# Kernel optimization log

Measured on AMD Instinct MI355X. Metric: run time of the kernel, lower is better.

The kernel has to match this reference:

```python
import jax, jax.numpy as jnp
import numpy as np

HIDDEN = 1024
INTER = 2048
NUM_EXPERTS = 8
TOP_K = 2
GROUP_SIZE = 128
TOKENS = 4096


def _dequant_int4(packed, scale, group_size):
    # packed: [E, N, K//2] ints in [0,256) holding two uint4 nibbles (low | high<<4)
    # scale:  [E, N, K//group_size] float32
    E, N, Kh = packed.shape
    K = 2 * Kh
    low = packed & 0xF
    high = (packed >> 4) & 0xF
    # interleave: even K positions = low nibble, odd = high nibble
    q = jnp.stack([low, high], axis=-1).reshape(E, N, K) - 8  # int4 values in [-8,7]
    q = q.astype(jnp.float32).reshape(E, N, K // group_size, group_size)
    w = q * scale[..., None]
    return w.reshape(E, N, K)


def setup_inputs() -> dict:
    key = jax.random.key(0)
    k1, k2, k3, k4, k5, k6 = jax.random.split(key, 6)
    x = jax.random.normal(k1, (TOKENS, HIDDEN), dtype=jnp.float32)
    router_w = jax.random.normal(k2, (NUM_EXPERTS, HIDDEN), dtype=jnp.float32) * 0.02
    w1 = jax.random.randint(k3, (NUM_EXPERTS, 2 * INTER, HIDDEN // 2), 0, 256, dtype=jnp.int32)
    w1_scale = jax.random.uniform(k4, (NUM_EXPERTS, 2 * INTER, HIDDEN // GROUP_SIZE), dtype=jnp.float32) * 0.05
    w2 = jax.random.randint(k5, (NUM_EXPERTS, HIDDEN, INTER // 2), 0, 256, dtype=jnp.int32)
    w2_scale = jax.random.uniform(k6, (NUM_EXPERTS, HIDDEN, INTER // GROUP_SIZE), dtype=jnp.float32) * 0.05
    return {"x": x, "router_w": router_w, "w1": w1, "w1_scale": w1_scale, "w2": w2, "w2_scale": w2_scale}


def reference(x, router_w, w1, w1_scale, w2, w2_scale):
    # Router: topk then softmax over the top-k logits
    scores = x @ router_w.T                                 # [T, E]
    top_w, top_i = jax.lax.top_k(scores, TOP_K)             # [T, K]
    top_w = jax.nn.softmax(top_w, axis=-1).astype(jnp.float32)

    # Dequantize int4 grouped weights once
    w1_deq = _dequant_int4(w1, w1_scale, GROUP_SIZE)        # [E, 2I, H]
    w2_deq = _dequant_int4(w2, w2_scale, GROUP_SIZE)        # [E, H, I]

    out = jnp.zeros_like(x)
    for e in range(NUM_EXPERTS):
        # per-token routing weight for expert e (0 if not routed)
        ge = jnp.sum(top_w * (top_i == e), axis=-1)         # [T]
        h = x @ w1_deq[e].T                                  # [T, 2I]
        gate, up = h[:, :INTER], h[:, INTER:]
        a = jax.nn.silu(gate) * up                           # SwiGLU
        y = a @ w2_deq[e].T                                  # [T, H]
        out = out + ge[:, None] * y
    return out
```

## Files before the change

kernel.cpp:

```cpp
#include <hip/hip_runtime.h>
#include <hip/hip_bf16.h>

#define HIDDEN 1024
#define INTER 2048
#define NE 8
#define GS 128
#define TOKENS 4096
#define MAXROWS 9216
#define MAXTILES 72
#define MAXT256 40

typedef __bf16 bf16x8 __attribute__((ext_vector_type(8)));
typedef float f32x4 __attribute__((ext_vector_type(4)));

#define OFF_TOPKI 0u
#define OFF_TOPKW 32768u
#define OFF_CTRL  65536u
#define OFF_TOK   66048u
#define OFF_SLOT  102912u
#define OFF_TILE  135680u
#define OFF_T256  136192u
#define OFF_V256  136448u
#define OFF_XB    139776u
#define OFF_A     8530432u
#define OFF_Y0    46279168u
#define OFF_Y1    (OFF_Y0 + 18874368u)

__device__ __forceinline__ unsigned short f2bf(float f) {
  union { float f; unsigned int u; } v; v.f = f;
  unsigned int r = (v.u + 0x7FFFu + ((v.u >> 16) & 1u)) >> 16;
  return (unsigned short)r;
}
__device__ __forceinline__ float bf2f(unsigned int u) {
  union { unsigned int u; float f; } v; v.u = u << 16;
  return v.f;
}
__device__ __forceinline__ unsigned int pack2(unsigned short lo, unsigned short hi) {
  return (unsigned int)lo | ((unsigned int)hi << 16);
}

typedef const __attribute__((address_space(1))) unsigned int GAS;
typedef __attribute__((address_space(3))) unsigned int LAS;
__device__ __forceinline__ void gload16(const unsigned short* g, unsigned short* l) {
  __builtin_amdgcn_global_load_lds((GAS*)g, (LAS*)l, 16, 0, 0);
}

__device__ __forceinline__ uint4 deq8(int4 p, float s, float c) {
  unsigned int pv[4] = { (unsigned int)p.x, (unsigned int)p.y,
                         (unsigned int)p.z, (unsigned int)p.w };
  unsigned int ov[4];
#pragma unroll
  for (int j = 0; j < 4; j++) {
    unsigned int v = pv[j];
    float flo = __uint_as_float(0x43000000u | ((v & 15u) << 16));
    float fhi = __uint_as_float(0x43000000u | ((v << 12) & 0x000F0000u));
    float lo = __builtin_fmaf(flo, s, c);
    float hi = __builtin_fmaf(fhi, s, c);
    unsigned int pk;
    asm("v_cvt_pk_bf16_f32 %0, %1, %2" : "=v"(pk) : "v"(lo), "v"(hi));
    ov[j] = pk;
  }
  uint4 o; o.x = ov[0]; o.y = ov[1]; o.z = ov[2]; o.w = ov[3];
  return o;
}

__global__ __launch_bounds__(256) void k_prep(const float* __restrict__ x,
    const float* __restrict__ rw, int* __restrict__ topki, float* __restrict__ topkw,
    unsigned short* __restrict__ xb) {
  int bid = blockIdx.x, tid = threadIdx.x;
  if (bid == 1024) {
    uint2 z; z.x = 0u; z.y = 0u;
    *reinterpret_cast<uint2*>(xb + (size_t)TOKENS * HIDDEN + tid * 4) = z;
    return;
  }
  int wave = tid >> 6, lane = tid & 63;
  int t = bid * 4 + wave;
  const float* xr = x + (size_t)t * HIDDEN;
  float acc[NE];
#pragma unroll
  for (int e = 0; e < NE; e++) acc[e] = 0.f;
#pragma unroll
  for (int j = 0; j < 4; j++) {
    int col = j * 256 + lane * 4;
    float4 xv = *reinterpret_cast<const float4*>(xr + col);
    uint2 o;
    o.x = pack2(f2bf(xv.x), f2bf(xv.y));
    o.y = pack2(f2bf(xv.z), f2bf(xv.w));
    *reinterpret_cast<uint2*>(xb + (size_t)t * HIDDEN + col) = o;
#pragma unroll
    for (int e = 0; e < NE; e++) {
      float4 wv = *reinterpret_cast<const float4*>(rw + e * HIDDEN + col);
      acc[e] += xv.x * wv.x + xv.y * wv.y + xv.z * wv.z + xv.w * wv.w;
    }
  }
#pragma unroll
  for (int e = 0; e < NE; e++) {
    float v = acc[e];
    for (int off = 32; off > 0; off >>= 1) v += __shfl_down(v, off, 64);
    acc[e] = v;
  }
  if (lane == 0) {
    int b0 = 0; float s0 = acc[0];
#pragma unroll
    for (int e = 1; e < NE; e++) if (acc[e] > s0) { s0 = acc[e]; b0 = e; }
    int b1 = -1; float s1 = -3.0e38f;
#pragma unroll
    for (int e = 0; e < NE; e++) if (e != b0 && acc[e] > s1) { s1 = acc[e]; b1 = e; }
    float w0 = 1.f / (1.f + __expf(s1 - s0));
    topki[t * 2] = b0; topki[t * 2 + 1] = b1;
    topkw[t * 2] = w0; topkw[t * 2 + 1] = 1.f - w0;
  }
}

__global__ __launch_bounds__(256) void k_route2(const int* __restrict__ topki,
    int* __restrict__ ctrl, int* __restrict__ tok, int* __restrict__ slots,
    int* __restrict__ tilemap, int* __restrict__ tile256, int* __restrict__ valid256) {
  __shared__ int h[NE], off[NE], cnt[NE];
  int tid = threadIdx.x;
  if (tid < NE) h[tid] = 0;
  __syncthreads();
  for (int i = tid; i < TOKENS * 2; i += 256) atomicAdd(&h[topki[i]], 1);
  __syncthreads();
  if (tid == 0) {
    int run = 0, t = 0, t2 = 0;
    for (int e = 0; e < NE; e++) {
      int c = h[e];
      ctrl[e] = c; ctrl[16 + e] = run; off[e] = run;
      int pc = (c + 127) & ~127;
      int m = pc >> 7;
      for (int mt = 0; mt < m; mt++) tilemap[t++] = (e << 20) | (run + mt * 128);
      int n2 = (m + 1) >> 1;
      for (int i2 = 0; i2 < n2; i2++) {
        int st = i2 * 256;
        if (st + 256 > pc) st = (pc >= 256) ? (pc - 256) : 0;
        tile256[t2] = (e << 20) | (run + st);
        int v = pc - st; valid256[t2] = (v < 256) ? v : 256;
        t2++;
      }
      run += pc;
    }
    ctrl[24] = run; ctrl[25] = t; ctrl[26] = t2;
  }
  __syncthreads();
#pragma unroll
  for (int e = 0; e < NE; e++) {
    int c = h[e], pc = (c + 127) & ~127;
    for (int i = c + tid; i < pc; i += 256) tok[off[e] + i] = -1;
  }
  if (tid < NE) cnt[tid] = off[tid];
  __syncthreads();
  for (int i = tid; i < TOKENS * 2; i += 256) {
    int e = topki[i];
    int p = atomicAdd(&cnt[e], 1);
    tok[p] = i >> 1;
    slots[i] = p;
  }
}

__global__ __launch_bounds__(256) void k_gemm1(
    const unsigned short* __restrict__ xb, const int* __restrict__ w1,
    const float* __restrict__ w1s, const int* __restrict__ ctrl,
    const int* __restrict__ tilemap, const int* __restrict__ tok,
    unsigned short* __restrict__ a_out) {
  __shared__ unsigned short sA[128 * 32];
  __shared__ unsigned short sBg[64 * 32];
  __shared__ unsigned short sBu[64 * 32];
  int bid = blockIdx.x, tid = threadIdx.x;
  int nt = bid & 31, tile = bid >> 5;
  if (tile >= ctrl[25]) return;
  int tm = tilemap[tile];
  int e = tm >> 20, row0 = tm & 0xFFFFF;
  int n0 = nt * 64;
  int wave = tid >> 6, lane = tid & 63;
  int ln = lane & 15, quad = lane >> 4;
  int wr = (wave & 1) * 64, wc = (wave >> 1) * 32;

  int srow = tid >> 2;
  int gcb = (tid & 3) ^ ((srow >> 1) & 3);
  int scol = gcb * 8;
  int t0 = tok[row0 + srow];
  int t1 = tok[row0 + 64 + srow];
  const unsigned short* gA0 = xb + (size_t)(t0 < 0 ? TOKENS : t0) * HIDDEN + scol;
  const unsigned short* gA1 = xb + (size_t)(t1 < 0 ? TOKENS : t1) * HIDDEN + scol;
  const int* gPg = w1 + (((size_t)e * 4096 + n0 + srow) << 9) + gcb * 4;
  const int* gPu = gPg + ((size_t)2048 << 9);
  const float* sWg = w1s + ((size_t)e * 4096 + n0 + srow) * 8;
  const float* sWu = sWg + 2048 * 8;
  unsigned short* lA0 = sA + tid * 8;
  unsigned short* lA1 = sA + 64 * 32 + tid * 8;
  unsigned short* lBg = sBg + tid * 8;
  unsigned short* lBu = sBu + tid * 8;

  f32x4 aG[4][2] = {}, aU[4][2] = {};
  for (int g = 0; g < 8; g++) {
    float sg_ = sWg[g], su_ = sWu[g];
    float cg = -136.f * sg_, cu = -136.f * su_;
#pragma unroll
    for (int kk = 0; kk < 4; kk++) {
      int k0 = g * 128 + kk * 32;
      __syncthreads();
      gload16(gA0 + k0, lA0);
      gload16(gA1 + k0, lA1);
      int4 pg = *reinterpret_cast<const int4*>(gPg + (k0 >> 1));
      int4 pu = *reinterpret_cast<const int4*>(gPu + (k0 >> 1));
      *reinterpret_cast<uint4*>(lBg) = deq8(pg, sg_, cg);
      *reinterpret_cast<uint4*>(lBu) = deq8(pu, su_, cu);
      __syncthreads();
      bf16x8 af[4], bg[2], bu[2];
#pragma unroll
      for (int m = 0; m < 4; m++) {
        int ar = wr + m * 16 + ln;
        af[m] = *reinterpret_cast<const bf16x8*>(&sA[ar * 32 + (quad ^ ((ar >> 1) & 3)) * 8]);
      }
#pragma unroll
      for (int n = 0; n < 2; n++) {
        int br = wc + n * 16 + ln;
        int bo = br * 32 + (quad ^ ((br >> 1) & 3)) * 8;
        bg[n] = *reinterpret_cast<const bf16x8*>(&sBg[bo]);
        bu[n] = *reinterpret_cast<const bf16x8*>(&sBu[bo]);
      }
#pragma unroll
      for (int m = 0; m < 4; m++)
#pragma unroll
        for (int n = 0; n < 2; n++) {
          aG[m][n] = __builtin_amdgcn_mfma_f32_16x16x32_bf16(af[m], bg[n], aG[m][n], 0, 0, 0);
          aU[m][n] = __builtin_amdgcn_mfma_f32_16x16x32_bf16(af[m], bu[n], aU[m][n], 0, 0, 0);
        }
    }
  }
#pragma unroll
  for (int m = 0; m < 4; m++)
#pragma unroll
    for (int n = 0; n < 2; n++) {
      int col = n0 + wc + n * 16 + ln;
#pragma unroll
      for (int r = 0; r < 4; r++) {
        float g = aG[m][n][r], u = aU[m][n][r];
        float act = (g / (1.f + __expf(-g))) * u;
        int row = row0 + wr + m * 16 + quad * 4 + r;
        a_out[(size_t)row * INTER + col] = f2bf(act);
      }
    }
}

__global__ __launch_bounds__(256) void k_gemm2(
    const unsigned short* __restrict__ a_in, const int* __restrict__ w2,
    const float* __restrict__ w2s, const int* __restrict__ ctrl,
    const int* __restrict__ tilemap, unsigned short* __restrict__ y) {
  __shared__ unsigned short sA[128 * 32];
  __shared__ unsigned short sB[128 * 32];
  int bid = blockIdx.x, tid = threadIdx.x;
  int kp = bid & 1, nt = (bid >> 1) & 7, tile = bid >> 4;
  if (tile >= ctrl[25]) return;
  int tm = tilemap[tile];
  int e = tm >> 20, row0 = tm & 0xFFFFF;
  int n0 = nt * 128;
  int wave = tid >> 6, lane = tid & 63;
  int ln = lane & 15, quad = lane >> 4;
  int wr = (wave & 1) * 64, wc = (wave >> 1) * 64;

  int srow = tid >> 2;
  int gcb = (tid & 3) ^ ((srow >> 1) & 3);
  int scol = gcb * 8;
  int kbase = kp * (INTER / 2);
  const unsigned short* gA0 = a_in + (size_t)(row0 + srow) * INTER + kbase + scol;
  const unsigned short* gA1 = gA0 + (size_t)64 * INTER;
  const int* gP0 = w2 + ((size_t)e * 1024 + n0 + srow) * 1024 + (kbase >> 1) + gcb * 4;
  const int* gP1 = gP0 + (size_t)64 * 1024;
  const float* sW0 = w2s + ((size_t)e * 1024 + n0 + srow) * 16 + kp * 8;
  const float* sW1 = sW0 + 64 * 16;
  unsigned short* lA0 = sA + tid * 8;
  unsigned short* lA1 = sA + 64 * 32 + tid * 8;
  unsigned short* lB0 = sB + tid * 8;
  unsigned short* lB1 = sB + 64 * 32 + tid * 8;

  f32x4 acc[4][4] = {};
  for (int g = 0; g < 8; g++) {
    float s0_ = sW0[g], s1_ = sW1[g];
    float c0 = -136.f * s0_, c1 = -136.f * s1_;
#pragma unroll
    for (int kk = 0; kk < 4; kk++) {
      int k0 = g * 128 + kk * 32;
      __syncthreads();
      gload16(gA0 + k0, lA0);
      gload16(gA1 + k0, lA1);
      int4 p0 = *reinterpret_cast<const int4*>(gP0 + (k0 >> 1));
      int4 p1 = *reinterpret_cast<const int4*>(gP1 + (k0 >> 1));
      *reinterpret_cast<uint4*>(lB0) = deq8(p0, s0_, c0);
      *reinterpret_cast<uint4*>(lB1) = deq8(p1, s1_, c1);
      __syncthreads();
      bf16x8 af[4], bf_[4];
#pragma unroll
      for (int m = 0; m < 4; m++) {
        int ar = wr + m * 16 + ln;
        af[m] = *reinterpret_cast<const bf16x8*>(&sA[ar * 32 + (quad ^ ((ar >> 1) & 3)) * 8]);
      }
#pragma unroll
      for (int n = 0; n < 4; n++) {
        int br = wc + n * 16 + ln;
        bf_[n] = *reinterpret_cast<const bf16x8*>(&sB[br * 32 + (quad ^ ((br >> 1) & 3)) * 8]);
      }
#pragma unroll
      for (int m = 0; m < 4; m++)
#pragma unroll
        for (int n = 0; n < 4; n++)
          acc[m][n] = __builtin_amdgcn_mfma_f32_16x16x32_bf16(af[m], bf_[n], acc[m][n], 0, 0, 0);
    }
  }
  unsigned short* yk = y + (size_t)kp * MAXROWS * HIDDEN;
#pragma unroll
  for (int m = 0; m < 4; m++)
#pragma unroll
    for (int n = 0; n < 4; n++) {
      int col = n0 + wc + n * 16 + ln;
#pragma unroll
      for (int r = 0; r < 4; r++) {
        int row = row0 + wr + m * 16 + quad * 4 + r;
        yk[(size_t)row * HIDDEN + col] = f2bf(acc[m][n][r]);
      }
    }
}

__global__ __launch_bounds__(256) void k_combine(const unsigned short* __restrict__ y,
    const int* __restrict__ slots, const float* __restrict__ topkw,
    float* __restrict__ out) {
  int t = blockIdx.x;
  int c = threadIdx.x * 4;
  int s0 = slots[t * 2], s1 = slots[t * 2 + 1];
  float g0 = topkw[t * 2], g1 = topkw[t * 2 + 1];
  const unsigned short* y1 = y + (size_t)MAXROWS * HIDDEN;
  uint2 a0 = *reinterpret_cast<const uint2*>(y  + (size_t)s0 * HIDDEN + c);
  uint2 a1 = *reinterpret_cast<const uint2*>(y1 + (size_t)s0 * HIDDEN + c);
  uint2 b0 = *reinterpret_cast<const uint2*>(y  + (size_t)s1 * HIDDEN + c);
  uint2 b1 = *reinterpret_cast<const uint2*>(y1 + (size_t)s1 * HIDDEN + c);
  float4 o;
  o.x = g0 * (bf2f(a0.x & 0xffffu) + bf2f(a1.x & 0xffffu))
      + g1 * (bf2f(b0.x & 0xffffu) + bf2f(b1.x & 0xffffu));
  o.y = g0 * (bf2f(a0.x >> 16) + bf2f(a1.x >> 16))
      + g1 * (bf2f(b0.x >> 16) + bf2f(b1.x >> 16));
  o.z = g0 * (bf2f(a0.y & 0xffffu) + bf2f(a1.y & 0xffffu))
      + g1 * (bf2f(b0.y & 0xffffu) + bf2f(b1.y & 0xffffu));
  o.w = g0 * (bf2f(a0.y >> 16) + bf2f(a1.y >> 16))
      + g1 * (bf2f(b0.y >> 16) + bf2f(b1.y >> 16));
  *reinterpret_cast<float4*>(out + (size_t)t * HIDDEN + c) = o;
}

extern "C" void kernel_launch(void* const* d_in, const int* in_sizes, int n_in,
                              void* d_out, int out_size, void* d_ws, size_t ws_size,
                              hipStream_t stream) {
  const float* x   = (const float*)d_in[0];
  const float* rw  = (const float*)d_in[1];
  const int*   w1  = (const int*)d_in[2];
  const float* w1s = (const float*)d_in[3];
  const int*   w2  = (const int*)d_in[4];
  const float* w2s = (const float*)d_in[5];
  float* out = (float*)d_out;
  char* ws = (char*)d_ws;

  int*   topki = (int*)(ws + OFF_TOPKI);
  float* topkw = (float*)(ws + OFF_TOPKW);
  int*   ctrl  = (int*)(ws + OFF_CTRL);
  int*   tok   = (int*)(ws + OFF_TOK);
  int*   slots = (int*)(ws + OFF_SLOT);
  int*   tilemap = (int*)(ws + OFF_TILE);
  int*   tile256 = (int*)(ws + OFF_T256);
  int*   valid256 = (int*)(ws + OFF_V256);
  unsigned short* xb  = (unsigned short*)(ws + OFF_XB);
  unsigned short* a   = (unsigned short*)(ws + OFF_A);
  unsigned short* y   = (unsigned short*)(ws + OFF_Y0);

  k_prep<<<1025, 256, 0, stream>>>(x, rw, topki, topkw, xb);
  k_route2<<<1, 256, 0, stream>>>(topki, ctrl, tok, slots, tilemap, tile256, valid256);
  k_gemm1<<<32 * MAXTILES, 256, 0, stream>>>(xb, w1, w1s, ctrl, tilemap, tok, a);
  k_gemm2<<<16 * MAXTILES, 256, 0, stream>>>(a, w2, w2s, ctrl, tilemap, y);
  k_combine<<<TOKENS, 256, 0, stream>>>(y, slots, topkw, out);
}
```

Before: 399.5 us.

## Double-buffer LDS tiles in both expert GEMMs to overlap loads with MFMA

Both GEMM kernels now hold two LDS buffers per operand. Each iteration issues the global loads for the next K-slice, runs MFMAs on the current buffer, then dequantizes the prefetched int4 weights into the other buffer. This cuts the loop from two barriers per step to one and hides global-load latency behind compute. It doubles LDS use per block, which may lower occupancy, and on the last step it redundantly reloads the final slice.

```diff
diff --git a/kernel.cpp b/kernel.cpp
--- a/kernel.cpp
+++ b/kernel.cpp
@@ -162,9 +162,9 @@
     const float* __restrict__ w1s, const int* __restrict__ ctrl,
     const int* __restrict__ tilemap, const int* __restrict__ tok,
     unsigned short* __restrict__ a_out) {
-  __shared__ unsigned short sA[128 * 32];
-  __shared__ unsigned short sBg[64 * 32];
-  __shared__ unsigned short sBu[64 * 32];
+  __shared__ unsigned short sA[2 * 128 * 32];
+  __shared__ unsigned short sBg[2 * 64 * 32];
+  __shared__ unsigned short sBu[2 * 64 * 32];
   int bid = blockIdx.x, tid = threadIdx.x;
   int nt = bid & 31, tile = bid >> 5;
   if (tile >= ctrl[25]) return;
@@ -186,47 +186,54 @@
   const int* gPu = gPg + ((size_t)2048 << 9);
   const float* sWg = w1s + ((size_t)e * 4096 + n0 + srow) * 8;
   const float* sWu = sWg + 2048 * 8;
-  unsigned short* lA0 = sA + tid * 8;
-  unsigned short* lA1 = sA + 64 * 32 + tid * 8;
-  unsigned short* lBg = sBg + tid * 8;
-  unsigned short* lBu = sBu + tid * 8;
+
+  gload16(gA0, sA + tid * 8);
+  gload16(gA1, sA + 64 * 32 + tid * 8);
+  {
+    int4 pg = *reinterpret_cast<const int4*>(gPg);
+    int4 pu = *reinterpret_cast<const int4*>(gPu);
+    float sg_ = sWg[0], su_ = sWu[0];
+    *reinterpret_cast<uint4*>(sBg + tid * 8) = deq8(pg, sg_, -136.f * sg_);
+    *reinterpret_cast<uint4*>(sBu + tid * 8) = deq8(pu, su_, -136.f * su_);
+  }
+  __syncthreads();
 
   f32x4 aG[4][2] = {}, aU[4][2] = {};
-  for (int g = 0; g < 8; g++) {
-    float sg_ = sWg[g], su_ = sWu[g];
-    float cg = -136.f * sg_, cu = -136.f * su_;
-#pragma unroll
-    for (int kk = 0; kk < 4; kk++) {
-      int k0 = g * 128 + kk * 32;
-      __syncthreads();
-      gload16(gA0 + k0, lA0);
-      gload16(gA1 + k0, lA1);
-      int4 pg = *reinterpret_cast<const int4*>(gPg + (k0 >> 1));
-      int4 pu = *reinterpret_cast<const int4*>(gPu + (k0 >> 1));
-      *reinterpret_cast<uint4*>(lBg) = deq8(pg, sg_, cg);
-      *reinterpret_cast<uint4*>(lBu) = deq8(pu, su_, cu);
-      __syncthreads();
-      bf16x8 af[4], bg[2], bu[2];
-#pragma unroll
-      for (int m = 0; m < 4; m++) {
-        int ar = wr + m * 16 + ln;
-        af[m] = *reinterpret_cast<const bf16x8*>(&sA[ar * 32 + (quad ^ ((ar >> 1) & 3)) * 8]);
+  for (int kt = 0; kt < 32; kt++) {
+    int buf = kt & 1, nb = buf ^ 1;
+    int kn = (kt < 31) ? kt + 1 : kt;
+    int k1 = kn * 32;
+    gload16(gA0 + k1, sA + nb * 4096 + tid * 8);
+    gload16(gA1 + k1, sA + nb * 4096 + 64 * 32 + tid * 8);
+    int4 pg = *reinterpret_cast<const int4*>(gPg + (k1 >> 1));
+    int4 pu = *reinterpret_cast<const int4*>(gPu + (k1 >> 1));
+    float sg_ = sWg[kn >> 2], su_ = sWu[kn >> 2];
+    const unsigned short* Ab = sA + buf * 4096;
+    const unsigned short* Bg = sBg + buf * 2048;
+    const unsigned short* Bu = sBu + buf * 2048;
+    bf16x8 af[4], bg[2], bu[2];
+#pragma unroll
+    for (int m = 0; m < 4; m++) {
+      int ar = wr + m * 16 + ln;
+      af[m] = *reinterpret_cast<const bf16x8*>(&Ab[ar * 32 + (quad ^ ((ar >> 1) & 3)) * 8]);
+    }
+#pragma unroll
+    for (int n = 0; n < 2; n++) {
+      int br = wc + n * 16 + ln;
+      int bo = br * 32 + (quad ^ ((br >> 1) & 3)) * 8;
+      bg[n] = *reinterpret_cast<const bf16x8*>(&Bg[bo]);
+      bu[n] = *reinterpret_cast<const bf16x8*>(&Bu[bo]);
+    }
+#pragma unroll
+    for (int m = 0; m < 4; m++)
+#pragma unroll
+      for (int n = 0; n < 2; n++) {
+        aG[m][n] = __builtin_amdgcn_mfma_f32_16x16x32_bf16(af[m], bg[n], aG[m][n], 0, 0, 0);
+        aU[m][n] = __builtin_amdgcn_mfma_f32_16x16x32_bf16(af[m], bu[n], aU[m][n], 0, 0, 0);
       }
-#pragma unroll
-      for (int n = 0; n < 2; n++) {
-        int br = wc + n * 16 + ln;
-        int bo = br * 32 + (quad ^ ((br >> 1) & 3)) * 8;
-        bg[n] = *reinterpret_cast<const bf16x8*>(&sBg[bo]);
-        bu[n] = *reinterpret_cast<const bf16x8*>(&sBu[bo]);
-      }
-#pragma unroll
-      for (int m = 0; m < 4; m++)
-#pragma unroll
-        for (int n = 0; n < 2; n++) {
-          aG[m][n] = __builtin_amdgcn_mfma_f32_16x16x32_bf16(af[m], bg[n], aG[m][n], 0, 0, 0);
-          aU[m][n] = __builtin_amdgcn_mfma_f32_16x16x32_bf16(af[m], bu[n], aU[m][n], 0, 0, 0);
-        }
-    }
+    *reinterpret_cast<uint4*>(sBg + nb * 2048 + tid * 8) = deq8(pg, sg_, -136.f * sg_);
+    *reinterpret_cast<uint4*>(sBu + nb * 2048 + tid * 8) = deq8(pu, su_, -136.f * su_);
+    __syncthreads();
   }
 #pragma unroll
   for (int m = 0; m < 4; m++)
@@ -247,8 +254,8 @@
     const unsigned short* __restrict__ a_in, const int* __restrict__ w2,
     const float* __restrict__ w2s, const int* __restrict__ ctrl,
     const int* __restrict__ tilemap, unsigned short* __restrict__ y) {
-  __shared__ unsigned short sA[128 * 32];
-  __shared__ unsigned short sB[128 * 32];
+  __shared__ unsigned short sA[2 * 128 * 32];
+  __shared__ unsigned short sB[2 * 128 * 32];
   int bid = blockIdx.x, tid = threadIdx.x;
   int kp = bid & 1, nt = (bid >> 1) & 7, tile = bid >> 4;
   if (tile >= ctrl[25]) return;
@@ -269,43 +276,49 @@
   const int* gP1 = gP0 + (size_t)64 * 1024;
   const float* sW0 = w2s + ((size_t)e * 1024 + n0 + srow) * 16 + kp * 8;
   const float* sW1 = sW0 + 64 * 16;
-  unsigned short* lA0 = sA + tid * 8;
-  unsigned short* lA1 = sA + 64 * 32 + tid * 8;
-  unsigned short* lB0 = sB + tid * 8;
-  unsigned short* lB1 = sB + 64 * 32 + tid * 8;
+
+  gload16(gA0, sA + tid * 8);
+  gload16(gA1, sA + 64 * 32 + tid * 8);
+  {
+    int4 p0 = *reinterpret_cast<const int4*>(gP0);
+    int4 p1 = *reinterpret_cast<const int4*>(gP1);
+    float s0_ = sW0[0], s1_ = sW1[0];
+    *reinterpret_cast<uint4*>(sB + tid * 8) = deq8(p0, s0_, -136.f * s0_);
+    *reinterpret_cast<uint4*>(sB + 64 * 32 + tid * 8) = deq8(p1, s1_, -136.f * s1_);
+  }
+  __syncthreads();
 
   f32x4 acc[4][4] = {};
-  for (int g = 0; g < 8; g++) {
-    float s0_ = sW0[g], s1_ = sW1[g];
-    float c0 = -136.f * s0_, c1 = -136.f * s1_;
-#pragma unroll
-    for (int kk = 0; kk < 4; kk++) {
-      int k0 = g * 128 + kk * 32;
-      __syncthreads();
-      gload16(gA0 + k0, lA0);
-      gload16(gA1 + k0, lA1);
-      int4 p0 = *reinterpret_cast<const int4*>(gP0 + (k0 >> 1));
-      int4 p1 = *reinterpret_cast<const int4*>(gP1 + (k0 >> 1));
-      *reinterpret_cast<uint4*>(lB0) = deq8(p0, s0_, c0);
-      *reinterpret_cast<uint4*>(lB1) = deq8(p1, s1_, c1);
-      __syncthreads();
-      bf16x8 af[4], bf_[4];
-#pragma unroll
-      for (int m = 0; m < 4; m++) {
-        int ar = wr + m * 16 + ln;
-        af[m] = *reinterpret_cast<const bf16x8*>(&sA[ar * 32 + (quad ^ ((ar >> 1) & 3)) * 8]);
-      }
-#pragma unroll
-      for (int n = 0; n < 4; n++) {
-        int br = wc + n * 16 + ln;
-        bf_[n] = *reinterpret_cast<const bf16x8*>(&sB[br * 32 + (quad ^ ((br >> 1) & 3)) * 8]);
-      }
-#pragma unroll
-      for (int m = 0; m < 4; m++)
-#pragma unroll
-        for (int n = 0; n < 4; n++)
-          acc[m][n] = __builtin_amdgcn_mfma_f32_16x16x32_bf16(af[m], bf_[n], acc[m][n], 0, 0, 0);
-    }
+  for (int kt = 0; kt < 32; kt++) {
+    int buf = kt & 1, nb = buf ^ 1;
+    int kn = (kt < 31) ? kt + 1 : kt;
+    int k1 = kn * 32;
+    gload16(gA0 + k1, sA + nb * 4096 + tid * 8);
+    gload16(gA1 + k1, sA + nb * 4096 + 64 * 32 + tid * 8);
+    int4 p0 = *reinterpret_cast<const int4*>(gP0 + (k1 >> 1));
+    int4 p1 = *reinterpret_cast<const int4*>(gP1 + (k1 >> 1));
+    float s0_ = sW0[kn >> 2], s1_ = sW1[kn >> 2];
+    const unsigned short* Ab = sA + buf * 4096;
+    const unsigned short* Bb = sB + buf * 4096;
+    bf16x8 af[4], bf_[4];
+#pragma unroll
+    for (int m = 0; m < 4; m++) {
+      int ar = wr + m * 16 + ln;
+      af[m] = *reinterpret_cast<const bf16x8*>(&Ab[ar * 32 + (quad ^ ((ar >> 1) & 3)) * 8]);
+    }
+#pragma unroll
+    for (int n = 0; n < 4; n++) {
+      int br = wc + n * 16 + ln;
+      bf_[n] = *reinterpret_cast<const bf16x8*>(&Bb[br * 32 + (quad ^ ((br >> 1) & 3)) * 8]);
+    }
+#pragma unroll
+    for (int m = 0; m < 4; m++)
+#pragma unroll
+      for (int n = 0; n < 4; n++)
+        acc[m][n] = __builtin_amdgcn_mfma_f32_16x16x32_bf16(af[m], bf_[n], acc[m][n], 0, 0, 0);
+    *reinterpret_cast<uint4*>(sB + nb * 4096 + tid * 8) = deq8(p0, s0_, -136.f * s0_);
+    *reinterpret_cast<uint4*>(sB + nb * 4096 + 64 * 32 + tid * 8) = deq8(p1, s1_, -136.f * s1_);
+    __syncthreads();
   }
   unsigned short* yk = y + (size_t)kp * MAXROWS * HIDDEN;
 #pragma unroll
```

Result: no change. 400.9 us (+0.4%).
